# Performance work log

Measured on AMD Instinct MI355X. Metric: run time of the kernel, lower is better.

Reference implementation:

```python
import jax, jax.numpy as jnp
import numpy as np


def _conv(x, w, stride, dil):
    # VALID conv in NCHW / OIHW layout with rhs (kernel) dilation
    return jax.lax.conv_general_dilated(
        x, w, window_strides=stride, padding='VALID', rhs_dilation=dil,
        dimension_numbers=('NCHW', 'OIHW', 'NCHW'))


def setup_inputs() -> dict:
    key = jax.random.key(0)
    k1, k2, k3 = jax.random.split(key, 3)
    B, Cin, H, W = 8, 64, 256, 256  # W even => columns_mod2 == 0
    Cout = 128
    inp = jax.random.normal(k1, (B, Cin, H, W), dtype=jnp.float32)
    # kaiming-normal-style init as in the torch module
    fan0 = Cin * 3 * 1
    kernel0 = jax.random.normal(k2, (Cout, Cin, 3, 1), dtype=jnp.float32) * np.float32(np.sqrt(2.0 / fan0))
    fan1 = Cin * 2 * 2
    kernel1 = jax.random.normal(k3, (Cout, Cin, 2, 2), dtype=jnp.float32) * np.float32(np.sqrt(2.0 / fan1))
    bias = jnp.full((Cout,), 0.01, dtype=jnp.float32)
    return {'input': inp, 'kernel0': kernel0, 'kernel1': kernel1, 'bias': bias}


def reference(input, kernel0, kernel1, bias):
    # hexagdly conv2d, size=1, stride=1, even number of columns (columns_mod2 = 0)
    x = input
    # kernel0: vertical 3x1 stencil over all columns; bias added once here
    even_all = _conv(jnp.pad(x, ((0, 0), (0, 0), (1, 1), (0, 0))), kernel0, (1, 1), (1, 1))
    even_all = even_all + bias[None, :, None, None]
    # kernel1: 2x2 stencil with horizontal dilation 2, stride 2 in width,
    # with column-parity-dependent vertical offset (hex grid)
    # odd columns: ZeroPad2d(left=1, right=0, top=1, bottom=0)
    ooc = _conv(jnp.pad(x, ((0, 0), (0, 0), (1, 0), (1, 0))), kernel1, (1, 2), (1, 2))
    # even columns: ZeroPad2d(left=0, right=1, top=0, bottom=1)
    oec = _conv(jnp.pad(x, ((0, 0), (0, 0), (0, 1), (0, 1))), kernel1, (1, 2), (1, 2))
    # interleave columns: out[..., 2k] = ooc[..., k], out[..., 2k+1] = oec[..., k]
    B, C, H, Wh = ooc.shape
    inter = jnp.stack([ooc, oec], axis=-1).reshape(B, C, H, 2 * Wh)
    return even_all + inter
```

## Files before the change

kernel.cpp:

```cpp
#include <hip/hip_runtime.h>
#include <hip/hip_bf16.h>


#define CIN  64
#define COUT 128
#define HH   256
#define WW   256
#define TH   8
#define TW   32
#define XR   10
#define XC   34

typedef __attribute__((ext_vector_type(8))) short short8;
typedef __attribute__((ext_vector_type(4))) float f32x4;

static __device__ __forceinline__ unsigned short f2bf(float v) {
    __hip_bfloat16 h = __float2bfloat16(v);
    return __builtin_bit_cast(unsigned short, h);
}

typedef __attribute__((address_space(1))) const unsigned int asg_u32;
typedef __attribute__((address_space(3))) unsigned int asl_u32;
static __device__ __forceinline__ void gl2lds16(const void* g, void* l) {
    __builtin_amdgcn_global_load_lds((asg_u32*)g, (asl_u32*)l, 16, 0, 0);
}

#define XS_BYTES   (XR * XC * CIN * 2)
#define WTB_OFF    XS_BYTES
#define SMEM_BYTES (XS_BYTES + 2 * COUT * CIN * 2)
#define WTAP       (COUT * CIN)

__global__ __launch_bounds__(512)
void prep_weights(const float* __restrict__ k0, const float* __restrict__ k1,
                  unsigned short* __restrict__ wsw)
{
    const int idx = blockIdx.x * 512 + threadIdx.x;
    if (idx >= 7 * COUT * 8) return;
    const int t   = idx >> 10;
    const int co  = (idx >> 3) & 127;
    const int ci0 = (idx & 7) * 8;
    short8 wv;
    #pragma unroll
    for (int j = 0; j < 8; ++j) {
        const int ci = ci0 + j;
        float v = (t < 3) ? k0[(co * CIN + ci) * 3 + t]
                          : k1[(co * CIN + ci) * 4 + (t - 3)];
        wv[j] = (short)f2bf(v);
    }
    const int e = (co * CIN + ci0) ^ ((co & 7) * 8);
    *(short8*)&wsw[t * WTAP + e] = wv;
}

__global__ __launch_bounds__(512, 4)
void hexconv_mfma(const float* __restrict__ x,
                  const unsigned short* __restrict__ wsw,
                  const float* __restrict__ bias,
                  float* __restrict__ out)
{
    __shared__ alignas(16) char smem[SMEM_BYTES];
    __shared__ float bias_lds[COUT];
    unsigned short* xs  = (unsigned short*)smem;
    unsigned short* wtb = (unsigned short*)(smem + WTB_OFF);

    const int tid  = threadIdx.x;
    const int lane = tid & 63;
    const int wid  = tid >> 6;

    const int wg = (blockIdx.x & 7) * 256 + (blockIdx.x >> 3);
    const int bx = wg & 7;
    const int by = (wg >> 3) & 31;
    const int b  = wg >> 8;

    const int h0 = by * TH;
    const int w0 = bx * TW;

    auto stage_tap = [&](int t, int buf) {
        const unsigned short* s0 = wsw + t * WTAP + wid * 1024;
        unsigned short* d0 = wtb + buf * WTAP + wid * 1024;
        gl2lds16(s0 + lane * 8, d0);
        gl2lds16(s0 + 512 + lane * 8, d0 + 512);
    };

    stage_tap(0, 0);

    if (tid < COUT) bias_lds[tid] = bias[tid];

    {
        const float* xb = x + (size_t)b * CIN * HH * WW;
        const int cg = tid & 7;
        const int u0 = tid >> 3;
        #pragma unroll
        for (int it = 0; it < 5; ++it) {
            const int u   = u0 + it * 64;
            const int row = u >> 5;
            const int ci  = (u & 31) * 2;
            const int gh  = h0 - 1 + row;
            f32x4 a = (f32x4)0.0f, c = (f32x4)0.0f;
            if ((unsigned)gh < HH) {
                const float* pb = xb + ((size_t)ci * HH + gh) * WW + w0 + 4 * cg;
                a = *(const f32x4*)pb;
                c = *(const f32x4*)(pb + HH * WW);
            }
            #pragma unroll
            for (int k = 0; k < 4; ++k) {
                const int col = 4 * cg + 1 + k;
                unsigned int pk = (unsigned int)f2bf(a[k]) | ((unsigned int)f2bf(c[k]) << 16);
                const int e = ((row * XC + col) * CIN + ci) ^ ((col & 7) * 8);
                *(unsigned int*)&xs[e] = pk;
            }
        }
        for (int i = tid; i < 2 * XR * CIN; i += 512) {
            const int side = (i >= XR * CIN) ? 1 : 0;
            const int rem  = i - side * XR * CIN;
            const int row  = rem >> 6;
            const int ci   = rem & 63;
            const int col  = side ? (XC - 1) : 0;
            const int gh   = h0 - 1 + row;
            const int gw   = side ? (w0 + TW) : (w0 - 1);
            float v = 0.f;
            if ((unsigned)gh < HH && (unsigned)gw < WW)
                v = xb[((size_t)ci * HH + gh) * WW + gw];
            const int e = ((row * XC + col) * CIN + ci) ^ ((col & 7) * 8);
            xs[e] = f2bf(v);
        }
    }

    __syncthreads();

    const int wm   = wid & 1;
    const int wn   = wid >> 1;
    const int c15  = lane & 15;
    const int q8   = (lane >> 4) * 8;
    const int par  = lane & 1;

    const int aBase = (wm * 64 + c15) * CIN + q8;
    const int swzA  = (c15 & 7) * 8;

    f32x4 acc[4][4];
    #pragma unroll
    for (int mi = 0; mi < 4; ++mi)
        #pragma unroll
        for (int ni = 0; ni < 4; ++ni)
            acc[mi][ni] = (f32x4)0.0f;

    #pragma unroll
    for (int tap = 0; tap < 7; ++tap) {
        if (tap < 6) {
            stage_tap(tap + 1, (tap + 1) & 1);
            asm volatile("s_waitcnt vmcnt(2)" ::: "memory");
        } else {
            asm volatile("s_waitcnt vmcnt(0)" ::: "memory");
        }
        __builtin_amdgcn_s_barrier();
        __builtin_amdgcn_sched_barrier(0);

        const unsigned short* wc = wtb + (tap & 1) * WTAP;

        int R0, P, C0;
        if (tap < 3) { R0 = tap; P = 0; C0 = 1; }
        else { R0 = (tap - 3) >> 1; P = 1; C0 = ((tap - 3) & 1) * 2; }
        const int colb  = c15 + C0;
        const int swzB  = (colb & 7) * 8;
        const int bBase = ((wn * 2 + R0 + P * par) * XC + colb) * CIN + q8;

        #pragma unroll
        for (int ci0 = 0; ci0 < CIN; ci0 += 32) {
            short8 af[4];
            #pragma unroll
            for (int mi = 0; mi < 4; ++mi)
                af[mi] = *(const short8*)&wc[(aBase + mi * 16 * CIN + ci0) ^ swzA];
            #pragma unroll
            for (int ni = 0; ni < 4; ++ni) {
                const int hr = ni >> 1, chalf = ni & 1;
                const int e = (bBase + hr * (XC * CIN) + chalf * (16 * CIN) + ci0) ^ swzB;
                short8 bf = *(const short8*)&xs[e];
                #pragma unroll
                for (int mi = 0; mi < 4; ++mi)
                    acc[mi][ni] = __builtin_amdgcn_mfma_f32_16x16x32_bf16(
                        af[mi], bf, acc[mi][ni], 0, 0, 0);
            }
        }

        asm volatile("s_waitcnt lgkmcnt(0)" ::: "memory");
        __builtin_amdgcn_sched_barrier(0);
        __builtin_amdgcn_s_barrier();
    }

    #pragma unroll
    for (int mi = 0; mi < 4; ++mi) {
        const int cobase = wm * 64 + mi * 16 + (lane >> 4) * 4;
        #pragma unroll
        for (int r = 0; r < 4; ++r) {
            const int co = cobase + r;
            const float bv = bias_lds[co];
            float* orow = out + ((size_t)b * COUT + co) * HH * WW;
            #pragma unroll
            for (int ni = 0; ni < 4; ++ni) {
                const int h = h0 + wn * 2 + (ni >> 1);
                const int w = w0 + (ni & 1) * 16 + c15;
                orow[(size_t)h * WW + w] = acc[mi][ni][r] + bv;
            }
        }
    }
}

extern "C" void kernel_launch(void* const* d_in, const int* in_sizes, int n_in,
                              void* d_out, int out_size, void* d_ws, size_t ws_size,
                              hipStream_t stream) {
    const float* x    = (const float*)d_in[0];
    const float* k0   = (const float*)d_in[1];
    const float* k1   = (const float*)d_in[2];
    const float* bias = (const float*)d_in[3];
    float* out        = (float*)d_out;
    unsigned short* wsw = (unsigned short*)d_ws;

    prep_weights<<<dim3(14, 1, 1), 512, 0, stream>>>(k0, k1, wsw);
    hexconv_mfma<<<dim3(2048, 1, 1), 512, 0, stream>>>(x, wsw, bias, out);
}
```

Measured before the change: 116.9 us.

## Split output channels across blocks, shrink tile, stage output through LDS

Each block now computes 64 output channels over an 8x16 spatial tile with 256 threads instead of 128 channels over 8x32 with 512 threads, so the grid grows to 8192 blocks. Weights are laid out per channel-half so each block stages only its half. The epilogue writes accumulators into padded LDS and then issues 16-byte nontemporal vector stores instead of scattered scalar stores. The input tile is now loaded twice (once per channel half), which adds global read traffic and per-block setup overhead in exchange for better occupancy and coalesced output writes.

```diff
diff --git a/kernel.cpp b/kernel.cpp
--- a/kernel.cpp
+++ b/kernel.cpp
@@ -2,14 +2,15 @@
 #include <hip/hip_bf16.h>
 
 
-#define CIN  64
-#define COUT 128
-#define HH   256
-#define WW   256
-#define TH   8
-#define TW   32
-#define XR   10
-#define XC   34
+#define CIN   64
+#define COUT  128
+#define COB   64
+#define HH    256
+#define WW    256
+#define TH    8
+#define TW    16
+#define XR    10
+#define XC    18
 
 typedef __attribute__((ext_vector_type(8))) short short8;
 typedef __attribute__((ext_vector_type(4))) float f32x4;
@@ -27,8 +28,9 @@
 
 #define XS_BYTES   (XR * XC * CIN * 2)
 #define WTB_OFF    XS_BYTES
-#define SMEM_BYTES (XS_BYTES + 2 * COUT * CIN * 2)
-#define WTAP       (COUT * CIN)
+#define SMEM_BYTES (XS_BYTES + 2 * COB * CIN * 2)
+#define OT_STRIDE  17
+#define WHALF      (COB * CIN)
 
 __global__ __launch_bounds__(512)
 void prep_weights(const float* __restrict__ k0, const float* __restrict__ k1,
@@ -36,59 +38,65 @@
 {
     const int idx = blockIdx.x * 512 + threadIdx.x;
     if (idx >= 7 * COUT * 8) return;
-    const int t   = idx >> 10;
-    const int co  = (idx >> 3) & 127;
-    const int ci0 = (idx & 7) * 8;
+    const int t    = idx >> 10;
+    const int rem  = idx & 1023;
+    const int chf  = rem >> 9;
+    const int co   = (rem >> 3) & 63;
+    const int ci0  = (idx & 7) * 8;
+    const int gco  = chf * 64 + co;
     short8 wv;
     #pragma unroll
     for (int j = 0; j < 8; ++j) {
         const int ci = ci0 + j;
-        float v = (t < 3) ? k0[(co * CIN + ci) * 3 + t]
-                          : k1[(co * CIN + ci) * 4 + (t - 3)];
+        float v = (t < 3) ? k0[(gco * CIN + ci) * 3 + t]
+                          : k1[(gco * CIN + ci) * 4 + (t - 3)];
         wv[j] = (short)f2bf(v);
     }
     const int e = (co * CIN + ci0) ^ ((co & 7) * 8);
-    *(short8*)&wsw[t * WTAP + e] = wv;
-}
-
-__global__ __launch_bounds__(512, 4)
+    *(short8*)&wsw[(t * 2 + chf) * WHALF + e] = wv;
+}
+
+__global__ __launch_bounds__(256, 4)
 void hexconv_mfma(const float* __restrict__ x,
                   const unsigned short* __restrict__ wsw,
                   const float* __restrict__ bias,
                   float* __restrict__ out)
 {
     __shared__ alignas(16) char smem[SMEM_BYTES];
-    __shared__ float bias_lds[COUT];
+    __shared__ float bias_lds[COB];
     unsigned short* xs  = (unsigned short*)smem;
     unsigned short* wtb = (unsigned short*)(smem + WTB_OFF);
+    float*          ot  = (float*)smem;
 
     const int tid  = threadIdx.x;
     const int lane = tid & 63;
     const int wid  = tid >> 6;
 
-    const int wg = (blockIdx.x & 7) * 256 + (blockIdx.x >> 3);
-    const int bx = wg & 7;
-    const int by = (wg >> 3) & 31;
-    const int b  = wg >> 8;
-
-    const int h0 = by * TH;
-    const int w0 = bx * TW;
+    const int wg  = (blockIdx.x & 7) * 1024 + (blockIdx.x >> 3);
+    const int chf = wg & 1;
+    const int bx  = (wg >> 1) & 15;
+    const int by  = (wg >> 5) & 31;
+    const int b   = wg >> 10;
+
+    const int co0 = chf * 64;
+    const int h0  = by * TH;
+    const int w0  = bx * TW;
 
     auto stage_tap = [&](int t, int buf) {
-        const unsigned short* s0 = wsw + t * WTAP + wid * 1024;
-        unsigned short* d0 = wtb + buf * WTAP + wid * 1024;
+        const unsigned short* s0 = wsw + (t * 2 + chf) * WHALF + wid * 1024;
+        unsigned short* d0 = wtb + buf * WHALF + wid * 1024;
         gl2lds16(s0 + lane * 8, d0);
         gl2lds16(s0 + 512 + lane * 8, d0 + 512);
     };
 
     stage_tap(0, 0);
 
-    if (tid < COUT) bias_lds[tid] = bias[tid];
+    if (tid < COB) bias_lds[tid] = bias[co0 + tid];
 
     {
         const float* xb = x + (size_t)b * CIN * HH * WW;
-        const int cg = tid & 7;
-        const int u0 = tid >> 3;
+        const int cg = tid & 3;
+        const int u0 = tid >> 2;
         #pragma unroll
         for (int it = 0; it < 5; ++it) {
             const int u   = u0 + it * 64;
@@ -109,7 +117,7 @@
                 *(unsigned int*)&xs[e] = pk;
             }
         }
-        for (int i = tid; i < 2 * XR * CIN; i += 512) {
+        for (int i = tid; i < 2 * XR * CIN; i += 256) {
             const int side = (i >= XR * CIN) ? 1 : 0;
             const int rem  = i - side * XR * CIN;
             const int row  = rem >> 6;
@@ -127,20 +135,19 @@
 
     __syncthreads();
 
-    const int wm   = wid & 1;
-    const int wn   = wid >> 1;
+    const int wn   = wid;
     const int c15  = lane & 15;
     const int q8   = (lane >> 4) * 8;
     const int par  = lane & 1;
 
-    const int aBase = (wm * 64 + c15) * CIN + q8;
+    const int aBase = c15 * CIN + q8;
     const int swzA  = (c15 & 7) * 8;
 
-    f32x4 acc[4][4];
+    f32x4 acc[4][2];
     #pragma unroll
     for (int mi = 0; mi < 4; ++mi)
         #pragma unroll
-        for (int ni = 0; ni < 4; ++ni)
+        for (int ni = 0; ni < 2; ++ni)
             acc[mi][ni] = (f32x4)0.0f;
 
     #pragma unroll
@@ -154,7 +161,7 @@
         __builtin_amdgcn_s_barrier();
         __builtin_amdgcn_sched_barrier(0);
 
-        const unsigned short* wc = wtb + (tap & 1) * WTAP;
+        const unsigned short* wc = wtb + (tap & 1) * WHALF;
 
         int R0, P, C0;
         if (tap < 3) { R0 = tap; P = 0; C0 = 1; }
@@ -170,9 +177,8 @@
             for (int mi = 0; mi < 4; ++mi)
                 af[mi] = *(const short8*)&wc[(aBase + mi * 16 * CIN + ci0) ^ swzA];
             #pragma unroll
-            for (int ni = 0; ni < 4; ++ni) {
-                const int hr = ni >> 1, chalf = ni & 1;
-                const int e = (bBase + hr * (XC * CIN) + chalf * (16 * CIN) + ci0) ^ swzB;
+            for (int ni = 0; ni < 2; ++ni) {
+                const int e = (bBase + ni * (XC * CIN) + ci0) ^ swzB;
                 short8 bf = *(const short8*)&xs[e];
                 #pragma unroll
                 for (int mi = 0; mi < 4; ++mi)
@@ -188,19 +194,30 @@
 
     #pragma unroll
     for (int mi = 0; mi < 4; ++mi) {
-        const int cobase = wm * 64 + mi * 16 + (lane >> 4) * 4;
-        #pragma unroll
-        for (int r = 0; r < 4; ++r) {
-            const int co = cobase + r;
-            const float bv = bias_lds[co];
-            float* orow = out + ((size_t)b * COUT + co) * HH * WW;
-            #pragma unroll
-            for (int ni = 0; ni < 4; ++ni) {
-                const int h = h0 + wn * 2 + (ni >> 1);
-                const int w = w0 + (ni & 1) * 16 + c15;
-                orow[(size_t)h * WW + w] = acc[mi][ni][r] + bv;
-            }
-        }
+        #pragma unroll
+        for (int ni = 0; ni < 2; ++ni) {
+            const int hh = wn * 2 + ni;
+            #pragma unroll
+            for (int r = 0; r < 4; ++r) {
+                const int col = mi * 16 + (lane >> 4) * 4 + r;
+                ot[(col * TH + hh) * OT_STRIDE + c15] =
+                    acc[mi][ni][r] + bias_lds[col];
+            }
+        }
+    }
+    asm volatile("s_waitcnt lgkmcnt(0)" ::: "memory");
+    __builtin_amdgcn_sched_barrier(0);
+    __builtin_amdgcn_s_barrier();
+    #pragma unroll
+    for (int it = 0; it < 8; ++it) {
+        const int idx = it * 256 + tid;
+        const int w4g = idx & 3;
+        const int hh  = (idx >> 2) & 7;
+        const int col = idx >> 5;
+        const float* src = &ot[(col * TH + hh) * OT_STRIDE + w4g * 4];
+        f32x4 v = { src[0], src[1], src[2], src[3] };
+        __builtin_nontemporal_store(v,
+            (f32x4*)&out[(((size_t)b * COUT + co0 + col) * HH + h0 + hh) * WW + w0 + w4g * 4]);
     }
 }
 
@@ -215,5 +232,5 @@
     unsigned short* wsw = (unsigned short*)d_ws;
 
     prep_weights<<<dim3(14, 1, 1), 512, 0, stream>>>(k0, k1, wsw);
-    hexconv_mfma<<<dim3(2048, 1, 1), 512, 0, stream>>>(x, wsw, bias, out);
-}
+    hexconv_mfma<<<dim3(8192, 1, 1), 256, 0, stream>>>(x, wsw, bias, out);
+}
```

Result: slower. 138.8 us (+18.7%).
